# Performance work log

Measured on AMD Instinct MI355X. Metric: run time of the kernel, lower is better.

Reference implementation:

```python
import jax, jax.numpy as jnp
import numpy as np

B, T, H, W, D = 2, 8, 32, 32, 256
NUM_HEADS, KWIN_K = 8, 3
LN_EPS = 1e-5


def build_neighbor_idx(h, w, k):
    # Matches _build_indices: for each of N=h*w positions, the k*k clamped
    # (replicate-padded) neighbor flat indices. Returned as [N, k*k]
    # (already permuted like `idx.permute(1, 0)` in the torch forward).
    r = k // 2
    hh, ww = np.meshgrid(np.arange(h), np.arange(w), indexing='ij')
    nbrs = []
    for dh in range(-r, r + 1):
        for dw in range(-r, r + 1):
            nh = np.clip(hh + dh, 0, h - 1)
            nw = np.clip(ww + dw, 0, w - 1)
            nbrs.append((nh * w + nw).reshape(-1))
    return jnp.asarray(np.stack(nbrs, axis=1), dtype=jnp.int32)  # [N, k*k]


def setup_inputs() -> dict:
    key = jax.random.key(0)
    ks = jax.random.split(key, 9)
    s = 1.0 / np.sqrt(D)
    return {
        'x': jax.random.normal(ks[0], (B, T, H, W, D), dtype=jnp.float32),
        'ln_g': jnp.ones((D,), jnp.float32),
        'ln_b': jnp.zeros((D,), jnp.float32),
        'wq': jax.random.normal(ks[1], (D, D), jnp.float32) * s,
        'bq': jax.random.normal(ks[2], (D,), jnp.float32) * 0.01,
        'wk': jax.random.normal(ks[3], (D, D), jnp.float32) * s,
        'bk': jax.random.normal(ks[4], (D,), jnp.float32) * 0.01,
        'wv': jax.random.normal(ks[5], (D, D), jnp.float32) * s,
        'bv': jax.random.normal(ks[6], (D,), jnp.float32) * 0.01,
        'wo': jax.random.normal(ks[7], (D, D), jnp.float32) * s,
        'bo': jax.random.normal(ks[8], (D,), jnp.float32) * 0.01,
    }


def reference(x, ln_g, ln_b, wq, bq, wk, bk, wv, bv, wo, bo):
    # Dropout layers are identity (inference mode).
    b, t, h, w, d = x.shape
    n = h * w
    hd = d // NUM_HEADS
    x_ = x.reshape(b * t, n, d)

    # LayerNorm over last dim
    mu = jnp.mean(x_, axis=-1, keepdims=True)
    var = jnp.var(x_, axis=-1, keepdims=True)
    xn = (x_ - mu) * jax.lax.rsqrt(var + LN_EPS) * ln_g + ln_b

    q = xn @ wq + bq
    k_ = xn @ wk + bk
    v = xn @ wv + bv

    def split_heads(tns):  # [BT, N, D] -> [BT, heads, N, hd]
        return tns.reshape(b * t, n, NUM_HEADS, hd).transpose(0, 2, 1, 3)

    qh, kh, vh = split_heads(q), split_heads(k_), split_heads(v)

    idx = build_neighbor_idx(h, w, KWIN_K)  # [N, Kwin]
    # Gather neighbors directly (no expand): [BT, heads, N, Kwin, hd]
    k_local = kh[:, :, idx, :]
    v_local = vh[:, :, idx, :]

    scores = jnp.einsum('bhnd,bhnkd->bhnk', qh, k_local) / np.sqrt(hd)
    attn = jax.nn.softmax(scores, axis=-1)
    out = jnp.einsum('bhnk,bhnkd->bhnd', attn, v_local)

    out = out.transpose(0, 2, 1, 3).reshape(b * t, n, d)
    out = out @ wo + bo
    out = out + x_
    return out.reshape(b, t, h, w, d)
```

## Files before the change

### kernel.cpp

```cpp
#include <hip/hip_runtime.h>
#include <hip/hip_bf16.h>

#define M_TOT 16384
#define D_    256
#define K_DIM 256

typedef __attribute__((ext_vector_type(4))) float f32x4;
typedef __attribute__((ext_vector_type(8))) short s16x8;
typedef __attribute__((ext_vector_type(4))) short s16x4;

typedef const __attribute__((address_space(1))) void* gptr_t;
typedef __attribute__((address_space(3))) void* lptr_t;

__device__ __forceinline__ unsigned short f2bf(float f) {
  unsigned x = __float_as_uint(f);
  return (unsigned short)((x + 0x7fffu + ((x >> 16) & 1u)) >> 16);
}
__device__ __forceinline__ float bf2f(short s) {
  return __uint_as_float(((unsigned)(unsigned short)s) << 16);
}

__global__ __launch_bounds__(256) void prep_kernel(
    const float* __restrict__ x, const float* __restrict__ g, const float* __restrict__ b,
    unsigned short* __restrict__ xn,
    const float* __restrict__ wq, const float* __restrict__ wk,
    const float* __restrict__ wv, const float* __restrict__ wo,
    unsigned short* __restrict__ wt_qkv, unsigned short* __restrict__ wt_o) {
  __shared__ float tile[32][33];
  int tid = threadIdx.x;
  if (blockIdx.x < 4096) {
    int tok  = blockIdx.x * 4 + (tid >> 6);
    int lane = tid & 63;
    f32x4 v = ((const f32x4*)(x + (size_t)tok * D_))[lane];
    float s = 0.f, s2 = 0.f;
#pragma unroll
    for (int i = 0; i < 4; ++i) { s += v[i]; s2 += v[i] * v[i]; }
#pragma unroll
    for (int o = 1; o < 64; o <<= 1) { s += __shfl_xor(s, o); s2 += __shfl_xor(s2, o); }
    float mu   = s * (1.0f / 256.0f);
    float rstd = rsqrtf(s2 * (1.0f / 256.0f) - mu * mu + 1e-5f);
    f32x4 gv = ((const f32x4*)g)[lane];
    f32x4 bv = ((const f32x4*)b)[lane];
    s16x4 o4;
#pragma unroll
    for (int i = 0; i < 4; ++i) o4[i] = (short)f2bf((v[i] - mu) * rstd * gv[i] + bv[i]);
    ((s16x4*)(xn + (size_t)tok * D_))[lane] = o4;
  } else {
    int bid = blockIdx.x - 4096;
    int z   = bid >> 6;
    int rem = bid & 63;
    int k0 = (rem & 7) * 32, n0 = (rem >> 3) * 32;
    int tx = tid & 31, ty = tid >> 5;
    const float* src = (z == 0) ? wq : (z == 1) ? wk : (z == 2) ? wv : wo;
#pragma unroll
    for (int i = 0; i < 4; ++i) {
      int r = ty + i * 8;
      tile[r][tx] = src[(size_t)(k0 + r) * D_ + n0 + tx];
    }
    __syncthreads();
    unsigned short* dst = (z < 3) ? (wt_qkv + (size_t)(z * 256 + n0) * K_DIM + k0)
                                  : (wt_o + (size_t)n0 * K_DIM + k0);
#pragma unroll
    for (int i = 0; i < 4; ++i) {
      int r = ty + i * 8;
      dst[(size_t)r * K_DIM + tx] = f2bf(tile[tx][r]);
    }
  }
}

__global__ __launch_bounds__(256) void gemm_qkv_kernel(
    const unsigned short* __restrict__ A, const unsigned short* __restrict__ Bt,
    const float* __restrict__ b0, const float* __restrict__ b1, const float* __restrict__ b2,
    unsigned short* __restrict__ C) {
  __shared__ __align__(16) char smem[32768];
  char* Asm = smem;
  char* Bsm = smem + 16384;
  const int tid  = threadIdx.x;
  const int wid  = tid >> 6;
  const int lane = tid & 63;
  int lin = blockIdx.y * 6 + blockIdx.x;
  int swz = (lin & 7) * 96 + (lin >> 3);
  const int m0 = (swz / 6) * 128;
  const int n0 = (swz % 6) * 128;
  const int wave_m = wid >> 1;
  const int wave_n = wid & 1;

  f32x4 acc[4][4] = {};

  for (int ks = 0; ks < 4; ++ks) {
    const int kk0 = ks * 64;
    __syncthreads();
#pragma unroll
    for (int it = 0; it < 4; ++it) {
      int base     = (it * 256 + wid * 64) * 16;
      int lane_lin = base + lane * 16;
      int row  = lane_lin >> 7;
      int off  = lane_lin & 127;
      int soff = off ^ ((row & 7) << 4);
      const char* ga = (const char*)(A + (size_t)(m0 + row) * K_DIM + kk0) + soff;
      const char* gb = (const char*)(Bt + (size_t)(n0 + row) * K_DIM + kk0) + soff;
      __builtin_amdgcn_global_load_lds((gptr_t)ga, (lptr_t)(Asm + base), 16, 0, 0);
      __builtin_amdgcn_global_load_lds((gptr_t)gb, (lptr_t)(Bsm + base), 16, 0, 0);
    }
    __syncthreads();

#pragma unroll
    for (int kk = 0; kk < 2; ++kk) {
      s16x8 af[4], bf[4];
#pragma unroll
      for (int m = 0; m < 4; ++m) {
        int r    = wave_m * 64 + m * 16 + (lane & 15);
        int byte = kk * 64 + ((lane >> 4) * 16);
        af[m] = *(const s16x8*)(Asm + r * 128 + (byte ^ ((r & 7) << 4)));
      }
#pragma unroll
      for (int n = 0; n < 4; ++n) {
        int r    = wave_n * 64 + n * 16 + (lane & 15);
        int byte = kk * 64 + ((lane >> 4) * 16);
        bf[n] = *(const s16x8*)(Bsm + r * 128 + (byte ^ ((r & 7) << 4)));
      }
#pragma unroll
      for (int m = 0; m < 4; ++m)
#pragma unroll
        for (int n = 0; n < 4; ++n)
          acc[m][n] = __builtin_amdgcn_mfma_f32_16x16x32_bf16(af[m], bf[n], acc[m][n], 0, 0, 0);
    }
  }

  const int c0 = lane & 15;
  const int r0 = (lane >> 4) * 4;
#pragma unroll
  for (int m = 0; m < 4; ++m) {
#pragma unroll
    for (int n = 0; n < 4; ++n) {
      int row = m0 + wave_m * 64 + m * 16 + r0;
      int col = n0 + wave_n * 64 + n * 16 + c0;
      const float* bias = (col < 256) ? b0 : (col < 512) ? b1 : b2;
      float bb = bias[col & 255];
#pragma unroll
      for (int r = 0; r < 4; ++r)
        C[(size_t)(row + r) * 768 + col] = f2bf(acc[m][n][r] + bb);
    }
  }
}

__global__ __launch_bounds__(512, 4) void attn_ogemm_kernel(
    const unsigned short* __restrict__ qkv, const unsigned short* __restrict__ wto,
    const float* __restrict__ bo, const float* __restrict__ x,
    float* __restrict__ out) {
  __shared__ __align__(16) char smem[65536];
  char* Halo = smem;
  char* Asm  = smem + 49152;
  const int tid  = threadIdx.x;
  const int wid  = tid >> 6;
  const int lane = tid & 63;
  int bswz = (blockIdx.x & 7) * 64 + (blockIdx.x >> 3);
  const int bt = bswz >> 5;
  const int h  = bswz & 31;
  const int t0 = bswz * 32;
  const size_t img = (size_t)bt << 10;

  int srow[3];
  srow[0] = max(h - 1, 0); srow[1] = h; srow[2] = min(h + 1, 31);

#pragma unroll
  for (int sweep = 0; sweep < 6; ++sweep) {
    int chunk = sweep * 8 + wid;
    int slot = chunk >> 4, t2 = chunk & 15;
    int tokw = t2 * 2 + (lane >> 5);
    int off  = (lane & 31) * 16;
    size_t grow = img + (size_t)srow[slot] * 32 + tokw;
    const char* ga = (const char*)qkv + grow * 1536 + 512 + off;
    __builtin_amdgcn_global_load_lds((gptr_t)ga, (lptr_t)(Halo + chunk * 1024), 16, 0, 0);
  }
  s16x4 qr4[4];
#pragma unroll
  for (int i = 0; i < 4; ++i)
    qr4[i] = *(const s16x4*)(qkv + (size_t)(t0 + wid * 4 + i) * 768 + lane * 4);
  s16x4 vreg[3][6];
#pragma unroll
  for (int s = 0; s < 3; ++s) {
#pragma unroll
    for (int cr = 0; cr < 6; ++cr) {
      int cc = min(max(wid * 4 - 1 + cr, 0), 31);
      vreg[s][cr] = *(const s16x4*)(qkv + (img + (size_t)srow[s] * 32 + cc) * 768 +
                                    512 + lane * 4);
    }
  }
  __syncthreads();

#pragma unroll
  for (int i = 0; i < 4; ++i) {
    int tloc = wid * 4 + i;
    f32x4 q;
#pragma unroll
    for (int e = 0; e < 4; ++e) q[e] = bf2f(qr4[i][e]);
    float sc[9];
#pragma unroll
    for (int s = 0; s < 3; ++s) {
#pragma unroll
      for (int dw = -1; dw <= 1; ++dw) {
        const int j = s * 3 + (dw + 1);
        int cw = min(max(tloc + dw, 0), 31);
        s16x4 kr = *(const s16x4*)(Halo + (s * 32 + cw) * 512 + lane * 8);
        float p = 0.f;
#pragma unroll
        for (int e = 0; e < 4; ++e) p += q[e] * bf2f(kr[e]);
        p += __shfl_xor(p, 1);
        p += __shfl_xor(p, 2);
        p += __shfl_xor(p, 4);
        sc[j] = p * 0.17677669529663687f;
      }
    }
    float mx = sc[0];
#pragma unroll
    for (int j = 1; j < 9; ++j) mx = fmaxf(mx, sc[j]);
    float den = 0.f;
#pragma unroll
    for (int j = 0; j < 9; ++j) { sc[j] = __expf(sc[j] - mx); den += sc[j]; }
    float inv = 1.0f / den;
    f32x4 o = {};
#pragma unroll
    for (int s = 0; s < 3; ++s) {
#pragma unroll
      for (int dw = -1; dw <= 1; ++dw) {
        const int j = s * 3 + (dw + 1);
        float wj = sc[j] * inv;
        s16x4 vr = vreg[s][i + dw + 1];
#pragma unroll
        for (int e = 0; e < 4; ++e) o[e] += wj * bf2f(vr[e]);
      }
    }
    s16x4 ov;
#pragma unroll
    for (int e = 0; e < 4; ++e) ov[e] = (short)f2bf(o[e]);
    int byte = (lane * 8) ^ ((tloc & 7) << 4);
    *(s16x4*)(Asm + tloc * 512 + byte) = ov;
  }

  const int wave_m = wid >> 2;
  const int wave_n = wid & 3;
  f32x4 acc[4] = {};

  for (int ks = 0; ks < 4; ++ks) {
    __syncthreads();
#pragma unroll
    for (int it = 0; it < 4; ++it) {
      int base     = it * 8192 + wid * 1024;
      int lane_lin = base + lane * 16;
      int row  = lane_lin >> 7;
      int off  = lane_lin & 127;
      int soff = off ^ ((row & 7) << 4);
      const char* gb = (const char*)(wto + (size_t)row * K_DIM + ks * 64) + soff;
      __builtin_amdgcn_global_load_lds((gptr_t)gb, (lptr_t)(Halo + base), 16, 0, 0);
    }
    __syncthreads();

#pragma unroll
    for (int kk = 0; kk < 2; ++kk) {
      s16x8 af, bf[4];
      {
        int r    = wave_m * 16 + (lane & 15);
        int byte = ks * 128 + kk * 64 + ((lane >> 4) * 16);
        af = *(const s16x8*)(Asm + r * 512 + (byte ^ ((r & 7) << 4)));
      }
#pragma unroll
      for (int n = 0; n < 4; ++n) {
        int r    = wave_n * 64 + n * 16 + (lane & 15);
        int byte = kk * 64 + ((lane >> 4) * 16);
        bf[n] = *(const s16x8*)(Halo + r * 128 + (byte ^ ((r & 7) << 4)));
      }
#pragma unroll
      for (int n = 0; n < 4; ++n)
        acc[n] = __builtin_amdgcn_mfma_f32_16x16x32_bf16(af, bf[n], acc[n], 0, 0, 0);
    }
  }

  const int c0 = lane & 15;
  const int r0 = (lane >> 4) * 4;
#pragma unroll
  for (int n = 0; n < 4; ++n) {
    int col = wave_n * 64 + n * 16 + c0;
    float bb = bo[col];
#pragma unroll
    for (int r = 0; r < 4; ++r) {
      int row = t0 + wave_m * 16 + r0 + r;
      out[(size_t)row * D_ + col] = acc[n][r] + bb + x[(size_t)row * D_ + col];
    }
  }
}

extern "C" void kernel_launch(void* const* d_in, const int* in_sizes, int n_in,
                              void* d_out, int out_size, void* d_ws, size_t ws_size,
                              hipStream_t stream) {
  const float* x  = (const float*)d_in[0];
  const float* lg = (const float*)d_in[1];
  const float* lb = (const float*)d_in[2];
  const float* wq = (const float*)d_in[3];
  const float* bq = (const float*)d_in[4];
  const float* wk = (const float*)d_in[5];
  const float* bk = (const float*)d_in[6];
  const float* wv = (const float*)d_in[7];
  const float* bv = (const float*)d_in[8];
  const float* wo = (const float*)d_in[9];
  const float* bo = (const float*)d_in[10];
  float* out = (float*)d_out;

  char* ws = (char*)d_ws;
  unsigned short* xn    = (unsigned short*)ws;
  unsigned short* qkv   = (unsigned short*)(ws + 8388608);
  unsigned short* wtqkv = (unsigned short*)(ws + 33554432);
  unsigned short* wto   = (unsigned short*)(ws + 33947648);

  prep_kernel<<<4352, 256, 0, stream>>>(x, lg, lb, xn, wq, wk, wv, wo, wtqkv, wto);
  gemm_qkv_kernel<<<dim3(6, 128), 256, 0, stream>>>(xn, wtqkv, bq, bk, bv, qkv);
  attn_ogemm_kernel<<<512, 512, 0, stream>>>(qkv, wto, bo, x, out);
}
```

Measured before the change: 41.20 us.

## Fuse LayerNorm into QKV GEMM A-tile loading, drop normalized activation buffer

LayerNorm is moved out of the prep kernel and into the QKV GEMM. Each block computes per-row mean and rstd for its 128 rows, then normalizes fp32 x on the fly into bf16 swizzled LDS A-tiles, while weight tiles still use async global-to-LDS loads. This removes the write and re-read of the bf16 xn buffer and the separate LN pass. In exchange, each of the 6 N-column blocks re-reads and re-normalizes the same fp32 rows, which adds global traffic (x read about 7 times in fp32) and VALU work, and the A loads are now synchronous register loads.

```diff
diff --git a/kernel.cpp b/kernel.cpp
--- a/kernel.cpp
+++ b/kernel.cpp
@@ -20,87 +20,107 @@
   return __uint_as_float(((unsigned)(unsigned short)s) << 16);
 }
 
-__global__ __launch_bounds__(256) void prep_kernel(
-    const float* __restrict__ x, const float* __restrict__ g, const float* __restrict__ b,
-    unsigned short* __restrict__ xn,
+__global__ __launch_bounds__(256) void wtrans_kernel(
     const float* __restrict__ wq, const float* __restrict__ wk,
     const float* __restrict__ wv, const float* __restrict__ wo,
     unsigned short* __restrict__ wt_qkv, unsigned short* __restrict__ wt_o) {
   __shared__ float tile[32][33];
   int tid = threadIdx.x;
-  if (blockIdx.x < 4096) {
-    int tok  = blockIdx.x * 4 + (tid >> 6);
-    int lane = tid & 63;
-    f32x4 v = ((const f32x4*)(x + (size_t)tok * D_))[lane];
-    float s = 0.f, s2 = 0.f;
-#pragma unroll
-    for (int i = 0; i < 4; ++i) { s += v[i]; s2 += v[i] * v[i]; }
-#pragma unroll
-    for (int o = 1; o < 64; o <<= 1) { s += __shfl_xor(s, o); s2 += __shfl_xor(s2, o); }
-    float mu   = s * (1.0f / 256.0f);
-    float rstd = rsqrtf(s2 * (1.0f / 256.0f) - mu * mu + 1e-5f);
-    f32x4 gv = ((const f32x4*)g)[lane];
-    f32x4 bv = ((const f32x4*)b)[lane];
-    s16x4 o4;
-#pragma unroll
-    for (int i = 0; i < 4; ++i) o4[i] = (short)f2bf((v[i] - mu) * rstd * gv[i] + bv[i]);
-    ((s16x4*)(xn + (size_t)tok * D_))[lane] = o4;
-  } else {
-    int bid = blockIdx.x - 4096;
-    int z   = bid >> 6;
-    int rem = bid & 63;
-    int k0 = (rem & 7) * 32, n0 = (rem >> 3) * 32;
-    int tx = tid & 31, ty = tid >> 5;
-    const float* src = (z == 0) ? wq : (z == 1) ? wk : (z == 2) ? wv : wo;
-#pragma unroll
-    for (int i = 0; i < 4; ++i) {
-      int r = ty + i * 8;
-      tile[r][tx] = src[(size_t)(k0 + r) * D_ + n0 + tx];
-    }
-    __syncthreads();
-    unsigned short* dst = (z < 3) ? (wt_qkv + (size_t)(z * 256 + n0) * K_DIM + k0)
-                                  : (wt_o + (size_t)n0 * K_DIM + k0);
-#pragma unroll
-    for (int i = 0; i < 4; ++i) {
-      int r = ty + i * 8;
-      dst[(size_t)r * K_DIM + tx] = f2bf(tile[tx][r]);
-    }
-  }
-}
-
-__global__ __launch_bounds__(256) void gemm_qkv_kernel(
-    const unsigned short* __restrict__ A, const unsigned short* __restrict__ Bt,
+  int bid = blockIdx.x;
+  int z   = bid >> 6;
+  int rem = bid & 63;
+  int k0 = (rem & 7) * 32, n0 = (rem >> 3) * 32;
+  int tx = tid & 31, ty = tid >> 5;
+  const float* src = (z == 0) ? wq : (z == 1) ? wk : (z == 2) ? wv : wo;
+#pragma unroll
+  for (int i = 0; i < 4; ++i) {
+    int r = ty + i * 8;
+    tile[r][tx] = src[(size_t)(k0 + r) * D_ + n0 + tx];
+  }
+  __syncthreads();
+  unsigned short* dst = (z < 3) ? (wt_qkv + (size_t)(z * 256 + n0) * K_DIM + k0)
+                                : (wt_o + (size_t)n0 * K_DIM + k0);
+#pragma unroll
+  for (int i = 0; i < 4; ++i) {
+    int r = ty + i * 8;
+    dst[(size_t)r * K_DIM + tx] = f2bf(tile[tx][r]);
+  }
+}
+
+__global__ __launch_bounds__(256) void lngemm_qkv_kernel(
+    const float* __restrict__ x, const float* __restrict__ g, const float* __restrict__ b,
+    const unsigned short* __restrict__ Bt,
     const float* __restrict__ b0, const float* __restrict__ b1, const float* __restrict__ b2,
     unsigned short* __restrict__ C) {
-  __shared__ __align__(16) char smem[32768];
-  char* Asm = smem;
-  char* Bsm = smem + 16384;
+  __shared__ __align__(16) char smem[36864];
+  char*  Asm  = smem;
+  char*  Bsm  = smem + 16384;
+  float* gbuf = (float*)(smem + 32768);
+  float* bbuf = (float*)(smem + 33792);
+  float* sbuf = (float*)(smem + 34816);
   const int tid  = threadIdx.x;
   const int wid  = tid >> 6;
   const int lane = tid & 63;
-  int lin = blockIdx.y * 6 + blockIdx.x;
+  int lin = blockIdx.x;
   int swz = (lin & 7) * 96 + (lin >> 3);
   const int m0 = (swz / 6) * 128;
   const int n0 = (swz % 6) * 128;
   const int wave_m = wid >> 1;
   const int wave_n = wid & 1;
 
+  gbuf[tid] = g[tid];
+  bbuf[tid] = b[tid];
+
+  {
+    int row = tid >> 1;
+    const f32x4* px = (const f32x4*)(x + (size_t)(m0 + row) * D_ + (tid & 1) * 128);
+    float s = 0.f, s2 = 0.f;
+#pragma unroll
+    for (int i = 0; i < 32; ++i) {
+      f32x4 v = px[i];
+#pragma unroll
+      for (int e = 0; e < 4; ++e) { s += v[e]; s2 += v[e] * v[e]; }
+    }
+    s  += __shfl_xor(s, 1);
+    s2 += __shfl_xor(s2, 1);
+    float mu   = s * (1.0f / 256.0f);
+    float rstd = rsqrtf(s2 * (1.0f / 256.0f) - mu * mu + 1e-5f);
+    if ((tid & 1) == 0) { sbuf[row * 2] = rstd; sbuf[row * 2 + 1] = -mu * rstd; }
+  }
+
   f32x4 acc[4][4] = {};
+  const int arow = tid >> 3;
+  const int acol = (tid & 7) * 8;
 
   for (int ks = 0; ks < 4; ++ks) {
     const int kk0 = ks * 64;
     __syncthreads();
 #pragma unroll
     for (int it = 0; it < 4; ++it) {
-      int base     = (it * 256 + wid * 64) * 16;
+      int base     = it * 4096 + wid * 1024;
       int lane_lin = base + lane * 16;
       int row  = lane_lin >> 7;
       int off  = lane_lin & 127;
       int soff = off ^ ((row & 7) << 4);
-      const char* ga = (const char*)(A + (size_t)(m0 + row) * K_DIM + kk0) + soff;
-      const char* gb = (const char*)(Bt + (size_t)(n0 + row) * K_DIM + kk0) + soff;
-      __builtin_amdgcn_global_load_lds((gptr_t)ga, (lptr_t)(Asm + base), 16, 0, 0);
-      __builtin_amdgcn_global_load_lds((gptr_t)gb, (lptr_t)(Bsm + base), 16, 0, 0);
+      const char* gb2 = (const char*)(Bt + (size_t)(n0 + row) * K_DIM + kk0) + soff;
+      __builtin_amdgcn_global_load_lds((gptr_t)gb2, (lptr_t)(Bsm + base), 16, 0, 0);
+    }
+#pragma unroll
+    for (int j = 0; j < 4; ++j) {
+      int r = j * 32 + arow;
+      float rstd = sbuf[r * 2], negc = sbuf[r * 2 + 1];
+      const float* px = x + (size_t)(m0 + r) * D_ + kk0 + acol;
+      f32x4 v0 = *(const f32x4*)px;
+      f32x4 v1 = *(const f32x4*)(px + 4);
+      const float* pg = gbuf + kk0 + acol;
+      const float* pb = bbuf + kk0 + acol;
+      s16x8 o8;
+#pragma unroll
+      for (int e = 0; e < 4; ++e) {
+        o8[e]     = (short)f2bf(fmaf(fmaf(v0[e], rstd, negc), pg[e], pb[e]));
+        o8[e + 4] = (short)f2bf(fmaf(fmaf(v1[e], rstd, negc), pg[e + 4], pb[e + 4]));
+      }
+      *(s16x8*)(Asm + r * 128 + ((acol * 2) ^ ((r & 7) << 4))) = o8;
     }
     __syncthreads();
 
@@ -307,12 +327,11 @@
   float* out = (float*)d_out;
 
   char* ws = (char*)d_ws;
-  unsigned short* xn    = (unsigned short*)ws;
   unsigned short* qkv   = (unsigned short*)(ws + 8388608);
   unsigned short* wtqkv = (unsigned short*)(ws + 33554432);
   unsigned short* wto   = (unsigned short*)(ws + 33947648);
 
-  prep_kernel<<<4352, 256, 0, stream>>>(x, lg, lb, xn, wq, wk, wv, wo, wtqkv, wto);
-  gemm_qkv_kernel<<<dim3(6, 128), 256, 0, stream>>>(xn, wtqkv, bq, bk, bv, qkv);
+  wtrans_kernel<<<256, 256, 0, stream>>>(wq, wk, wv, wo, wtqkv, wto);
+  lngemm_qkv_kernel<<<768, 256, 0, stream>>>(x, lg, lb, wtqkv, bq, bk, bv, qkv);
   attn_ogemm_kernel<<<512, 512, 0, stream>>>(qkv, wto, bo, x, out);
 }
```

Measured after the change: 56.68 us. +37.6%, slower.

## Split fused attention+output GEMM blocks into half-rows with 18-column K halo

Applied to the files above, without the earlier changes.

The fused attention/output-projection kernel now processes 16 tokens (half an image row) per 256-thread block instead of 32 tokens per 512-thread block, doubling the grid to 1024 blocks. The K halo shrinks to 3x18 columns, LDS drops from 64KB to 40KB to allow more resident blocks, and the residual x and output bias are prefetched into registers before the attention phase. The cost is that each block reloads the full Wo matrix for only 16 rows, doubling Wo traffic per token, and halo columns are duplicated across the two half-row blocks.

```diff
diff --git a/kernel.cpp b/kernel.cpp
--- a/kernel.cpp
+++ b/kernel.cpp
@@ -144,34 +144,41 @@
   }
 }
 
-__global__ __launch_bounds__(512, 4) void attn_ogemm_kernel(
+__global__ __launch_bounds__(256, 4) void attn_ogemm_kernel(
     const unsigned short* __restrict__ qkv, const unsigned short* __restrict__ wto,
     const float* __restrict__ bo, const float* __restrict__ x,
     float* __restrict__ out) {
-  __shared__ __align__(16) char smem[65536];
-  char* Halo = smem;
-  char* Asm  = smem + 49152;
+  __shared__ __align__(16) char smem[40960];
+  char* KB  = smem;
+  char* Asm = smem + 32768;
   const int tid  = threadIdx.x;
   const int wid  = tid >> 6;
   const int lane = tid & 63;
-  int bswz = (blockIdx.x & 7) * 64 + (blockIdx.x >> 3);
-  const int bt = bswz >> 5;
-  const int h  = bswz & 31;
-  const int t0 = bswz * 32;
+  int bswz = (blockIdx.x & 7) * 128 + (blockIdx.x >> 3);
+  const int imgrow = bswz >> 1;
+  const int half   = bswz & 1;
+  const int bt = imgrow >> 5;
+  const int h  = imgrow & 31;
+  const int w0 = half * 16;
+  const int t0 = imgrow * 32 + w0;
   const size_t img = (size_t)bt << 10;
 
   int srow[3];
   srow[0] = max(h - 1, 0); srow[1] = h; srow[2] = min(h + 1, 31);
 
-#pragma unroll
-  for (int sweep = 0; sweep < 6; ++sweep) {
-    int chunk = sweep * 8 + wid;
-    int slot = chunk >> 4, t2 = chunk & 15;
-    int tokw = t2 * 2 + (lane >> 5);
-    int off  = (lane & 31) * 16;
-    size_t grow = img + (size_t)srow[slot] * 32 + tokw;
-    const char* ga = (const char*)qkv + grow * 1536 + 512 + off;
-    __builtin_amdgcn_global_load_lds((gptr_t)ga, (lptr_t)(Halo + chunk * 1024), 16, 0, 0);
+  for (int sweep = 0; sweep < 7; ++sweep) {
+    int wl = sweep * 4 + wid;
+    if (wl < 27) {
+      int slot = wl / 9;
+      int pair = wl % 9;
+      int cp   = pair * 2 + (lane >> 5);
+      int gc   = min(max(w0 - 1 + cp, 0), 31);
+      int off  = (lane & 31) * 16;
+      size_t grow = img + (size_t)srow[slot] * 32 + gc;
+      const char* ga = (const char*)qkv + grow * 1536 + 512 + off;
+      __builtin_amdgcn_global_load_lds((gptr_t)ga,
+          (lptr_t)(KB + (slot * 18 + pair * 2) * 512), 16, 0, 0);
+    }
   }
   s16x4 qr4[4];
 #pragma unroll
@@ -182,16 +189,28 @@
   for (int s = 0; s < 3; ++s) {
 #pragma unroll
     for (int cr = 0; cr < 6; ++cr) {
-      int cc = min(max(wid * 4 - 1 + cr, 0), 31);
+      int cc = min(max(w0 + wid * 4 - 1 + cr, 0), 31);
       vreg[s][cr] = *(const s16x4*)(qkv + (img + (size_t)srow[s] * 32 + cc) * 768 +
                                     512 + lane * 4);
     }
   }
+  const int ec0 = lane & 15;
+  const int er0 = (lane >> 4) * 4;
+  float xv[4][4], bbv[4];
+#pragma unroll
+  for (int n = 0; n < 4; ++n) {
+    int col = wid * 64 + n * 16 + ec0;
+    bbv[n] = bo[col];
+#pragma unroll
+    for (int r = 0; r < 4; ++r)
+      xv[n][r] = x[(size_t)(t0 + er0 + r) * D_ + col];
+  }
   __syncthreads();
 
 #pragma unroll
   for (int i = 0; i < 4; ++i) {
-    int tloc = wid * 4 + i;
+    int wl_ = wid * 4 + i;
+    int w   = w0 + wl_;
     f32x4 q;
 #pragma unroll
     for (int e = 0; e < 4; ++e) q[e] = bf2f(qr4[i][e]);
@@ -201,8 +220,9 @@
 #pragma unroll
       for (int dw = -1; dw <= 1; ++dw) {
         const int j = s * 3 + (dw + 1);
-        int cw = min(max(tloc + dw, 0), 31);
-        s16x4 kr = *(const s16x4*)(Halo + (s * 32 + cw) * 512 + lane * 8);
+        int cw = min(max(w + dw, 0), 31);
+        int cp = cw - w0 + 1;
+        s16x4 kr = *(const s16x4*)(KB + (s * 18 + cp) * 512 + lane * 8);
         float p = 0.f;
 #pragma unroll
         for (int e = 0; e < 4; ++e) p += q[e] * bf2f(kr[e]);
@@ -234,25 +254,23 @@
     s16x4 ov;
 #pragma unroll
     for (int e = 0; e < 4; ++e) ov[e] = (short)f2bf(o[e]);
-    int byte = (lane * 8) ^ ((tloc & 7) << 4);
-    *(s16x4*)(Asm + tloc * 512 + byte) = ov;
-  }
-
-  const int wave_m = wid >> 2;
-  const int wave_n = wid & 3;
+    int byte = (lane * 8) ^ ((wl_ & 7) << 4);
+    *(s16x4*)(Asm + wl_ * 512 + byte) = ov;
+  }
+
   f32x4 acc[4] = {};
 
   for (int ks = 0; ks < 4; ++ks) {
     __syncthreads();
 #pragma unroll
-    for (int it = 0; it < 4; ++it) {
-      int base     = it * 8192 + wid * 1024;
+    for (int it = 0; it < 8; ++it) {
+      int base     = it * 4096 + wid * 1024;
       int lane_lin = base + lane * 16;
       int row  = lane_lin >> 7;
       int off  = lane_lin & 127;
       int soff = off ^ ((row & 7) << 4);
       const char* gb = (const char*)(wto + (size_t)row * K_DIM + ks * 64) + soff;
-      __builtin_amdgcn_global_load_lds((gptr_t)gb, (lptr_t)(Halo + base), 16, 0, 0);
+      __builtin_amdgcn_global_load_lds((gptr_t)gb, (lptr_t)(KB + base), 16, 0, 0);
     }
     __syncthreads();
 
@@ -260,15 +278,15 @@
     for (int kk = 0; kk < 2; ++kk) {
       s16x8 af, bf[4];
       {
-        int r    = wave_m * 16 + (lane & 15);
+        int r    = lane & 15;
         int byte = ks * 128 + kk * 64 + ((lane >> 4) * 16);
         af = *(const s16x8*)(Asm + r * 512 + (byte ^ ((r & 7) << 4)));
       }
 #pragma unroll
       for (int n = 0; n < 4; ++n) {
-        int r    = wave_n * 64 + n * 16 + (lane & 15);
+        int r    = wid * 64 + n * 16 + (lane & 15);
         int byte = kk * 64 + ((lane >> 4) * 16);
-        bf[n] = *(const s16x8*)(Halo + r * 128 + (byte ^ ((r & 7) << 4)));
+        bf[n] = *(const s16x8*)(KB + r * 128 + (byte ^ ((r & 7) << 4)));
       }
 #pragma unroll
       for (int n = 0; n < 4; ++n)
@@ -276,16 +294,13 @@
     }
   }
 
-  const int c0 = lane & 15;
-  const int r0 = (lane >> 4) * 4;
 #pragma unroll
   for (int n = 0; n < 4; ++n) {
-    int col = wave_n * 64 + n * 16 + c0;
-    float bb = bo[col];
+    int col = wid * 64 + n * 16 + ec0;
 #pragma unroll
     for (int r = 0; r < 4; ++r) {
-      int row = t0 + wave_m * 16 + r0 + r;
-      out[(size_t)row * D_ + col] = acc[n][r] + bb + x[(size_t)row * D_ + col];
+      int row = t0 + er0 + r;
+      out[(size_t)row * D_ + col] = acc[n][r] + bbv[n] + xv[n][r];
     }
   }
 }
@@ -314,5 +329,5 @@
 
   prep_kernel<<<4352, 256, 0, stream>>>(x, lg, lb, xn, wq, wk, wv, wo, wtqkv, wto);
   gemm_qkv_kernel<<<dim3(6, 128), 256, 0, stream>>>(xn, wtqkv, bq, bk, bv, qkv);
-  attn_ogemm_kernel<<<512, 512, 0, stream>>>(qkv, wto, bo, x, out);
-}
+  attn_ogemm_kernel<<<1024, 256, 0, stream>>>(qkv, wto, bo, x, out);
+}
```

New measurement: 44.44 us. 7.8% more time.

## Load output-projection weights directly into registers with double buffering

Applied to the files above, without the earlier changes.

Replaces the staged LDS copy of the output-projection weight tile (global_load_lds plus two barriers per k-step) with direct global-to-register loads. The loads are double buffered across the four k-steps, and the first load is issued before the attention phase so its latency overlaps that compute. This removes seven block-wide barriers and the LDS round trip for the B operand. In exchange it adds register pressure (16 s16x8 buffers) under launch_bounds(512,4), and each wave now fetches the weights from global or L2 without sharing through LDS.

```diff
diff --git a/kernel.cpp b/kernel.cpp
--- a/kernel.cpp
+++ b/kernel.cpp
@@ -144,6 +144,30 @@
   }
 }
 
+template <int KS>
+__device__ __forceinline__ void load_b(const unsigned short* __restrict__ wto,
+                                       int brow, int bcol, s16x8* buf) {
+#pragma unroll
+  for (int n = 0; n < 4; ++n)
+#pragma unroll
+    for (int kk = 0; kk < 2; ++kk)
+      buf[n * 2 + kk] = *(const s16x8*)(wto + (size_t)(brow + n * 16) * K_DIM +
+                                        KS * 64 + kk * 32 + bcol);
+}
+template <int KS>
+__device__ __forceinline__ void comp_b(const char* Asm, int wave_m, int lane,
+                                       const s16x8* buf, f32x4* acc) {
+#pragma unroll
+  for (int kk = 0; kk < 2; ++kk) {
+    int r    = wave_m * 16 + (lane & 15);
+    int byte = KS * 128 + kk * 64 + ((lane >> 4) * 16);
+    s16x8 af = *(const s16x8*)(Asm + r * 512 + (byte ^ ((r & 7) << 4)));
+#pragma unroll
+    for (int n = 0; n < 4; ++n)
+      acc[n] = __builtin_amdgcn_mfma_f32_16x16x32_bf16(af, buf[n * 2 + kk], acc[n], 0, 0, 0);
+  }
+}
+
 __global__ __launch_bounds__(512, 4) void attn_ogemm_kernel(
     const unsigned short* __restrict__ qkv, const unsigned short* __restrict__ wto,
     const float* __restrict__ bo, const float* __restrict__ x,
@@ -187,6 +211,12 @@
                                     512 + lane * 4);
     }
   }
+  const int wave_m = wid >> 2;
+  const int wave_n = wid & 3;
+  const int brow = wave_n * 64 + (lane & 15);
+  const int bcol = (lane >> 4) * 8;
+  s16x8 bufA[8], bufB[8];
+  load_b<0>(wto, brow, bcol, bufA);
   __syncthreads();
 
 #pragma unroll
@@ -237,44 +267,16 @@
     int byte = (lane * 8) ^ ((tloc & 7) << 4);
     *(s16x4*)(Asm + tloc * 512 + byte) = ov;
   }
-
-  const int wave_m = wid >> 2;
-  const int wave_n = wid & 3;
+  __syncthreads();
+
   f32x4 acc[4] = {};
-
-  for (int ks = 0; ks < 4; ++ks) {
-    __syncthreads();
-#pragma unroll
-    for (int it = 0; it < 4; ++it) {
-      int base     = it * 8192 + wid * 1024;
-      int lane_lin = base + lane * 16;
-      int row  = lane_lin >> 7;
-      int off  = lane_lin & 127;
-      int soff = off ^ ((row & 7) << 4);
-      const char* gb = (const char*)(wto + (size_t)row * K_DIM + ks * 64) + soff;
-      __builtin_amdgcn_global_load_lds((gptr_t)gb, (lptr_t)(Halo + base), 16, 0, 0);
-    }
-    __syncthreads();
-
-#pragma unroll
-    for (int kk = 0; kk < 2; ++kk) {
-      s16x8 af, bf[4];
-      {
-        int r    = wave_m * 16 + (lane & 15);
-        int byte = ks * 128 + kk * 64 + ((lane >> 4) * 16);
-        af = *(const s16x8*)(Asm + r * 512 + (byte ^ ((r & 7) << 4)));
-      }
-#pragma unroll
-      for (int n = 0; n < 4; ++n) {
-        int r    = wave_n * 64 + n * 16 + (lane & 15);
-        int byte = kk * 64 + ((lane >> 4) * 16);
-        bf[n] = *(const s16x8*)(Halo + r * 128 + (byte ^ ((r & 7) << 4)));
-      }
-#pragma unroll
-      for (int n = 0; n < 4; ++n)
-        acc[n] = __builtin_amdgcn_mfma_f32_16x16x32_bf16(af, bf[n], acc[n], 0, 0, 0);
-    }
-  }
+  load_b<1>(wto, brow, bcol, bufB);
+  comp_b<0>(Asm, wave_m, lane, bufA, acc);
+  load_b<2>(wto, brow, bcol, bufA);
+  comp_b<1>(Asm, wave_m, lane, bufB, acc);
+  load_b<3>(wto, brow, bcol, bufB);
+  comp_b<2>(Asm, wave_m, lane, bufA, acc);
+  comp_b<3>(Asm, wave_m, lane, bufB, acc);
 
   const int c0 = lane & 15;
   const int r0 = (lane >> 4) * 4;
```

Result: slower. 53.51 us (+29.9%).
